# Kernel tuning notes

Hardware: AMD Instinct MI355X
Metric: run time of the kernel (lower is better)

## Reference

```python
import jax, jax.numpy as jnp
import numpy as np

HIDDEN = 1024
HEADS = 16
B, L = 2, 2048


def _xavier(key, shape):
    fan_in, fan_out = shape[1], shape[0]
    limit = float(np.sqrt(6.0 / (fan_in + fan_out)))
    return jax.random.uniform(key, shape, jnp.float32, -limit, limit)


def setup_inputs() -> dict:
    key = jax.random.key(0)
    ks = jax.random.split(key, 6)
    return {
        "query": jax.random.normal(ks[0], (B, L, HIDDEN), jnp.float32),
        "bias": jax.random.normal(ks[1], (B, 1, 1, L), jnp.float32),
        "Wq": _xavier(ks[2], (HIDDEN, HIDDEN)), "bq": jnp.zeros((HIDDEN,), jnp.float32),
        "Wk": _xavier(ks[3], (HIDDEN, HIDDEN)), "bk": jnp.zeros((HIDDEN,), jnp.float32),
        "Wv": _xavier(ks[4], (HIDDEN, HIDDEN)), "bv": jnp.zeros((HIDDEN,), jnp.float32),
        "Wo": _xavier(ks[5], (HIDDEN, HIDDEN)), "bo": jnp.zeros((HIDDEN,), jnp.float32),
    }


def _split_heads(x):
    b, l, c = x.shape
    return x.reshape(b, l, HEADS, c // HEADS).transpose(0, 2, 1, 3)  # [B,H,L,d]


def reference(query, bias, Wq, bq, Wk, bk, Wv, bv, Wo, bo):
    d_head = HIDDEN // HEADS
    q = query @ Wq.T + bq
    k = query @ Wk.T + bk
    v = query @ Wv.T + bv
    q = _split_heads(q) * (d_head ** -0.5)  # [B,H,L,d]
    k = _split_heads(k)
    v = _split_heads(v)
    logits = jnp.einsum("bhqd,bhkd->bhqk", q, k) + bias  # [B,H,L,L]
    weights = jax.nn.softmax(logits, axis=-1)
    x = jnp.einsum("bhqk,bhkd->bhqd", weights, v)  # [B,H,L,d]
    x = x.transpose(0, 2, 1, 3).reshape(query.shape[0], query.shape[1], HIDDEN)
    return x @ Wo.T + bo
```

## Files before the change

### kernel.cpp

```cpp
#include <hip/hip_runtime.h>
#include <hip/hip_fp16.h>
#include <stdint.h>

#define HIDDEN 1024
#define HEADS  16
#define DH     64
#define B_     2
#define L_     2048
#define M_TOT  (B_ * L_)
#define ELEMS  (M_TOT * HIDDEN)
#define LOG2E  1.44269504088896340736f

typedef _Float16 f16;
typedef _Float16 f16x4 __attribute__((ext_vector_type(4)));
typedef _Float16 f16x8 __attribute__((ext_vector_type(8)));
typedef float    f32x4 __attribute__((ext_vector_type(4)));
typedef uint32_t u32;
typedef __attribute__((address_space(1))) u32 gu32;
typedef __attribute__((address_space(3))) u32 su32;

#define MFMA32(a, b, c) __builtin_amdgcn_mfma_f32_16x16x32_f16(a, b, c, 0, 0, 0)


__global__ __launch_bounds__(256)
void convert_f16(const float* __restrict__ query,
                 const float* __restrict__ Wq, const float* __restrict__ Wk,
                 const float* __restrict__ Wv, const float* __restrict__ Wo,
                 f16* __restrict__ Qh, f16* __restrict__ Wh)
{
    const int NQ4 = ELEMS / 4;
    const int NW4 = (HIDDEN * HIDDEN) / 4;
    const int total = NQ4 + 4 * NW4;
    for (int u = blockIdx.x * 256 + threadIdx.x; u < total; u += gridDim.x * 256) {
        float4 v; f16* dp;
        if (u < NQ4) {
            v = ((const float4*)query)[u];
            dp = Qh + (size_t)u * 4;
        } else {
            const int u2 = u - NQ4;
            const int w = u2 >> 18;
            const int off = u2 & (NW4 - 1);
            const float* W = (w == 0) ? Wq : (w == 1) ? Wk : (w == 2) ? Wv : Wo;
            v = ((const float4*)W)[off];
            dp = Wh + (size_t)u2 * 4;
        }
        f16x4 h = { (f16)v.x, (f16)v.y, (f16)v.z, (f16)v.w };
        *(f16x4*)dp = h;
    }
}

template<int TM, int TN>
__device__ __forceinline__
void gemm_loop(const f16* __restrict__ A, const f16* __restrict__ W,
               int mb, int nb, f32x4 (&acc)[TM / 32][TN / 32])
{
    __shared__ f16 As[3][TM * 32];
    __shared__ f16 Bs[3][TN * 32];

    const int tid  = threadIdx.x;
    const int lane = tid & 63;
    const int wave = tid >> 6;
    const int quad = lane >> 4;
    const int l16  = lane & 15;
    const int wm   = (wave >> 1) * (TM / 2);
    const int wn   = (wave & 1) * (TN / 2);

    constexpr int AISS = TM / 64;
    constexpr int BISS = TN / 64;
    int aoff[AISS], boff[BISS];
#pragma unroll
    for (int q = 0; q < AISS; q++) {
        const int p16 = (wave * AISS + q) * 64 + lane;
        const int r = p16 >> 2;
        const int c8 = (p16 & 3) ^ ((r >> 1) & 3);
        aoff[q] = (mb + r) * HIDDEN + c8 * 8;
    }
#pragma unroll
    for (int q = 0; q < BISS; q++) {
        const int p16 = (wave * BISS + q) * 64 + lane;
        const int r = p16 >> 2;
        const int c8 = (p16 & 3) ^ ((r >> 1) & 3);
        boff[q] = (nb + r) * HIDDEN + c8 * 8;
    }

#pragma unroll
    for (int p = 0; p < 2; p++) {
#pragma unroll
        for (int q = 0; q < AISS; q++)
            __builtin_amdgcn_global_load_lds((gu32*)&A[aoff[q] + p * 32],
                                             (su32*)&As[p][(wave * AISS + q) * 512], 16, 0, 0);
#pragma unroll
        for (int q = 0; q < BISS; q++)
            __builtin_amdgcn_global_load_lds((gu32*)&W[boff[q] + p * 32],
                                             (su32*)&Bs[p][(wave * BISS + q) * 512], 16, 0, 0);
    }

    int sl = 0;
#pragma unroll 1
    for (int kb = 0; kb < HIDDEN; kb += 32) {
        if constexpr (AISS + BISS == 4)
            asm volatile("s_waitcnt vmcnt(4)" ::: "memory");
        else
            asm volatile("s_waitcnt vmcnt(3)" ::: "memory");
        __builtin_amdgcn_s_barrier();
        __builtin_amdgcn_sched_barrier(0);

        const int nkb = (kb + 64 < HIDDEN) ? kb + 64 : 0;
        const int si  = (sl >= 1) ? sl - 1 : 2;
#pragma unroll
        for (int q = 0; q < AISS; q++)
            __builtin_amdgcn_global_load_lds((gu32*)&A[aoff[q] + nkb],
                                             (su32*)&As[si][(wave * AISS + q) * 512], 16, 0, 0);
#pragma unroll
        for (int q = 0; q < BISS; q++)
            __builtin_amdgcn_global_load_lds((gu32*)&W[boff[q] + nkb],
                                             (su32*)&Bs[si][(wave * BISS + q) * 512], 16, 0, 0);

        f16x8 af[TM / 32], bf[TN / 32];
#pragma unroll
        for (int i = 0; i < TM / 32; i++) {
            const int r = wm + i * 16 + l16;
            af[i] = *(const f16x8*)&As[sl][r * 32 + (quad ^ ((r >> 1) & 3)) * 8];
        }
#pragma unroll
        for (int j = 0; j < TN / 32; j++) {
            const int r = wn + j * 16 + l16;
            bf[j] = *(const f16x8*)&Bs[sl][r * 32 + (quad ^ ((r >> 1) & 3)) * 8];
        }
#pragma unroll
        for (int i = 0; i < TM / 32; i++)
#pragma unroll
            for (int j = 0; j < TN / 32; j++)
                acc[i][j] = MFMA32(af[i], bf[j], acc[i][j]);

        sl = (sl + 1 == 3) ? 0 : sl + 1;
    }
    asm volatile("s_waitcnt vmcnt(0)" ::: "memory");
}

__global__ __launch_bounds__(256)
void proj_qkv(const f16* __restrict__ A, const f16* __restrict__ W,
              const float* __restrict__ bq, const float* __restrict__ bk,
              const float* __restrict__ bv,
              f16* __restrict__ Qo, f16* __restrict__ Ko, f16* __restrict__ Vo)
{
    f32x4 acc[4][4] = {};
    const int mb = blockIdx.x * 128, nb = blockIdx.y * 128;
    gemm_loop<128, 128>(A, W, mb, nb, acc);

    const int lane = threadIdx.x & 63, wave = threadIdx.x >> 6;
    const int quad = lane >> 4, l16 = lane & 15;
    const int wm = (wave >> 1) * 64, wn = (wave & 1) * 64;
    const int nsel = nb >> 10;
    const int nbase = nb & 1023;

    if (nsel < 2) {
        const float* bias = nsel ? bk : bq;
        f16* out = nsel ? Ko : Qo;
        const float scale = nsel ? 1.0f : 0.125f * LOG2E;
#pragma unroll
        for (int i = 0; i < 4; i++)
#pragma unroll
            for (int j = 0; j < 4; j++) {
                const int n1 = nbase + wn + j * 16 + l16;
                const float bn = bias[n1];
                const int h = n1 >> 6, dd = n1 & 63;
#pragma unroll
                for (int r = 0; r < 4; r++) {
                    const int m = mb + wm + i * 16 + quad * 4 + r;
                    const int b = m >> 11, l = m & (L_ - 1);
                    out[(((b * HEADS + h) * L_) + l) * DH + dd] =
                        (f16)((acc[i][j][r] + bn) * scale);
                }
            }
    } else {
#pragma unroll
        for (int i = 0; i < 4; i++)
#pragma unroll
            for (int j = 0; j < 4; j++) {
                const int n1 = nbase + wn + j * 16 + l16;
                const float bn = bv[n1];
                const int h = n1 >> 6, dd = n1 & 63;
                const int m0 = mb + wm + i * 16 + quad * 4;
                const int b = m0 >> 11, l0 = m0 & (L_ - 1);
                f16x4 pk;
#pragma unroll
                for (int r = 0; r < 4; r++) pk[r] = (f16)(acc[i][j][r] + bn);
                *(f16x4*)&Vo[((size_t)(b * HEADS + h) * DH + dd) * L_ + l0] = pk;
            }
    }
}

__global__ __launch_bounds__(256)
void proj_out(const f16* __restrict__ A, const f16* __restrict__ W,
              const float* __restrict__ bo, float* __restrict__ out)
{
    f32x4 acc[4][2] = {};
    const int mb = blockIdx.x * 128, nb = blockIdx.y * 64;
    gemm_loop<128, 64>(A, W, mb, nb, acc);

    const int lane = threadIdx.x & 63, wave = threadIdx.x >> 6;
    const int quad = lane >> 4, l16 = lane & 15;
    const int wm = (wave >> 1) * 64, wn = (wave & 1) * 32;
#pragma unroll
    for (int i = 0; i < 4; i++)
#pragma unroll
        for (int j = 0; j < 2; j++) {
            const int n = nb + wn + j * 16 + l16;
            const float bn = bo[n];
#pragma unroll
            for (int r = 0; r < 4; r++) {
                const int m = mb + wm + i * 16 + quad * 4 + r;
                out[m * HIDDEN + n] = acc[i][j][r] + bn;
            }
        }
}

__global__ __launch_bounds__(256)
void attn(const f16* __restrict__ Q, const f16* __restrict__ K,
          const f16* __restrict__ Vt, const float* __restrict__ bias,
          f16* __restrict__ X)
{
    __shared__ f16 Ks[2][64 * 64];
    __shared__ f16 Vs[2][64 * 64];
    __shared__ float biasl[L_];

    const int tid  = threadIdx.x;
    const int lane = tid & 63;
    const int wave = tid >> 6;
    const int quad = lane >> 4;
    const int l16  = lane & 15;

    const int bid = (int)blockIdx.x;
    const int lb  = (bid & 7) * 128 + (bid >> 3);
    const int bh = lb >> 5;
    const int b  = bh >> 4, h = bh & 15;
    const int qrow0 = (lb & 31) * 64 + wave * 16;

    const f16* Qh  = Q  + (size_t)bh * L_ * DH;
    const f16* Kh  = K  + (size_t)bh * L_ * DH;
    const f16* Vth = Vt + (size_t)bh * DH * L_;

    {
        const float4* bb = (const float4*)(bias + b * L_);
        for (int i = tid; i < L_ / 4; i += 256) {
            const float4 v = bb[i];
            biasl[i * 4 + 0] = v.x * LOG2E;
            biasl[i * 4 + 1] = v.y * LOG2E;
            biasl[i * 4 + 2] = v.z * LOG2E;
            biasl[i * 4 + 3] = v.w * LOG2E;
        }
    }

    int krow[2], kcol[2], vcol[2];
#pragma unroll
    for (int q = 0; q < 2; q++) {
        const int p = (wave * 2 + q) * 64 + lane;
        const int r = p >> 3;
        const int w = p & 7;
        krow[q] = r;
        kcol[q] = (w ^ (r & 7) ^ (((r >> 3) & 1) << 2)) * 8;
        vcol[q] = (w ^ (r & 7)) * 8;
    }

    f16x8 qf[2];
#pragma unroll
    for (int hh = 0; hh < 2; hh++)
        qf[hh] = *(const f16x8*)&Qh[(qrow0 + l16) * DH + hh * 32 + quad * 8];

    int koffX[2][2], koffY[2][2], voff[2][4];
#pragma unroll
    for (int g = 0; g < 2; g++) {
        const int rX = g * 32 + ((l16 >> 2) << 3) + (l16 & 3);
        const int rY = rX + 4;
        const int gkX = (rX & 7) ^ (((rX >> 3) & 1) << 2);
        const int gkY = (rY & 7) ^ (((rY >> 3) & 1) << 2);
#pragma unroll
        for (int hh = 0; hh < 2; hh++) {
            koffX[g][hh] = rX * 64 + (((hh * 4 + quad) ^ gkX) << 3);
            koffY[g][hh] = rY * 64 + (((hh * 4 + quad) ^ gkY) << 3);
        }
#pragma unroll
        for (int t = 0; t < 4; t++) {
            const int vr = t * 16 + l16;
            voff[g][t] = vr * 64 + (((g * 4 + quad) ^ (vr & 7)) << 3);
        }
    }

#pragma unroll
    for (int q = 0; q < 2; q++) {
        __builtin_amdgcn_global_load_lds((gu32*)(Kh + (size_t)krow[q] * DH + kcol[q]),
                                         (su32*)&Ks[0][(wave * 2 + q) * 512], 16, 0, 0);
        __builtin_amdgcn_global_load_lds((gu32*)(Vth + (size_t)krow[q] * L_ + vcol[q]),
                                         (su32*)&Vs[0][(wave * 2 + q) * 512], 16, 0, 0);
    }

    f32x4 o[4] = {};
    f32x4 osum = {};
    const f16x8 ones8 = { (f16)1.f, (f16)1.f, (f16)1.f, (f16)1.f,
                          (f16)1.f, (f16)1.f, (f16)1.f, (f16)1.f };
    __syncthreads();

#pragma unroll 1
    for (int kb = 0; kb < L_; kb += 64) {
        const int buf = (kb >> 6) & 1;
        const int nkb = (kb + 64 < L_) ? kb + 64 : 0;

#pragma unroll
        for (int q = 0; q < 2; q++) {
            __builtin_amdgcn_global_load_lds(
                (gu32*)(Kh + (size_t)(nkb + krow[q]) * DH + kcol[q]),
                (su32*)&Ks[buf ^ 1][(wave * 2 + q) * 512], 16, 0, 0);
            __builtin_amdgcn_global_load_lds(
                (gu32*)(Vth + (size_t)krow[q] * L_ + nkb + vcol[q]),
                (su32*)&Vs[buf ^ 1][(wave * 2 + q) * 512], 16, 0, 0);
        }

#pragma unroll
        for (int g = 0; g < 2; g++) {
            const f16x8 kx0 = *(const f16x8*)&Ks[buf][koffX[g][0]];
            const f16x8 kx1 = *(const f16x8*)&Ks[buf][koffX[g][1]];
            const f16x8 ky0 = *(const f16x8*)&Ks[buf][koffY[g][0]];
            const f16x8 ky1 = *(const f16x8*)&Ks[buf][koffY[g][1]];
            f16x8 va[4];
#pragma unroll
            for (int t = 0; t < 4; t++)
                va[t] = *(const f16x8*)&Vs[buf][voff[g][t]];
            const f32x4 blvX = *(const f32x4*)&biasl[kb + g * 32 + quad * 8];
            const f32x4 blvY = *(const f32x4*)&biasl[kb + g * 32 + quad * 8 + 4];

            f32x4 zx = blvX, zy = blvY;
            zx = MFMA32(kx0, qf[0], zx);
            zx = MFMA32(kx1, qf[1], zx);
            zy = MFMA32(ky0, qf[0], zy);
            zy = MFMA32(ky1, qf[1], zy);
            const f16x8 pb = {
                (f16)__builtin_amdgcn_exp2f(zx[0]), (f16)__builtin_amdgcn_exp2f(zx[1]),
                (f16)__builtin_amdgcn_exp2f(zx[2]), (f16)__builtin_amdgcn_exp2f(zx[3]),
                (f16)__builtin_amdgcn_exp2f(zy[0]), (f16)__builtin_amdgcn_exp2f(zy[1]),
                (f16)__builtin_amdgcn_exp2f(zy[2]), (f16)__builtin_amdgcn_exp2f(zy[3]) };
#pragma unroll
            for (int t = 0; t < 4; t++)
                o[t] = MFMA32(va[t], pb, o[t]);
            osum = MFMA32(ones8, pb, osum);
        }
        __syncthreads();
    }

    {
        const float inv = 1.0f / osum[0];
        const size_t qrow = (size_t)b * L_ + qrow0 + l16;
#pragma unroll
        for (int t = 0; t < 4; t++) {
            f16x4 pk;
#pragma unroll
            for (int r = 0; r < 4; r++) pk[r] = (f16)(o[t][r] * inv);
            *(f16x4*)&X[qrow * HIDDEN + h * DH + t * 16 + quad * 4] = pk;
        }
    }
}

extern "C" void kernel_launch(void* const* d_in, const int* in_sizes, int n_in,
                              void* d_out, int out_size, void* d_ws, size_t ws_size,
                              hipStream_t stream)
{
    const float* query = (const float*)d_in[0];
    const float* bias  = (const float*)d_in[1];
    const float* Wq = (const float*)d_in[2]; const float* bq = (const float*)d_in[3];
    const float* Wk = (const float*)d_in[4]; const float* bk = (const float*)d_in[5];
    const float* Wv = (const float*)d_in[6]; const float* bv = (const float*)d_in[7];
    const float* Wo = (const float*)d_in[8]; const float* bo = (const float*)d_in[9];
    float* out = (float*)d_out;

    f16* Wh = (f16*)d_ws;
    f16* Qh = Wh + 4096 * 1024;
    f16* Kf = Qh + ELEMS;
    f16* Vf = Kf + ELEMS;
    f16* Qf = Vf + ELEMS;
    f16* Xf = Qh;

    convert_f16<<<2048, 256, 0, stream>>>(query, Wq, Wk, Wv, Wo, Qh, Wh);
    proj_qkv<<<dim3(32, 24), 256, 0, stream>>>(Qh, Wh, bq, bk, bv, Qf, Kf, Vf);
    attn<<<1024, 256, 0, stream>>>(Qf, Kf, Vf, bias, Xf);
    proj_out<<<dim3(32, 16), 256, 0, stream>>>(Xf, Wh + 3072 * 1024, bo, out);
}
```

Before: 201.4 us.

## Split attention keys across wave pairs with 2 query tiles each; vectorize GEMM epilogues

```diff
diff --git a/kernel.cpp b/kernel.cpp
--- a/kernel.cpp
+++ b/kernel.cpp
@@ -49,7 +49,7 @@
     }
 }
 
-template<int TM, int TN>
+template<int TM, int TN, bool SWAP>
 __device__ __forceinline__
 void gemm_loop(const f16* __restrict__ A, const f16* __restrict__ W,
                int mb, int nb, f32x4 (&acc)[TM / 32][TN / 32])
@@ -130,8 +130,12 @@
 #pragma unroll
         for (int i = 0; i < TM / 32; i++)
 #pragma unroll
-            for (int j = 0; j < TN / 32; j++)
-                acc[i][j] = MFMA32(af[i], bf[j], acc[i][j]);
+            for (int j = 0; j < TN / 32; j++) {
+                if constexpr (SWAP)
+                    acc[i][j] = MFMA32(bf[j], af[i], acc[i][j]);
+                else
+                    acc[i][j] = MFMA32(af[i], bf[j], acc[i][j]);
+            }
 
         sl = (sl + 1 == 3) ? 0 : sl + 1;
     }
@@ -146,12 +150,13 @@
 {
     f32x4 acc[4][4] = {};
     const int mb = blockIdx.x * 128, nb = blockIdx.y * 128;
-    gemm_loop<128, 128>(A, W, mb, nb, acc);
+    const int nsel = nb >> 10;
+    if (nsel < 2) gemm_loop<128, 128, true >(A, W, mb, nb, acc);
+    else          gemm_loop<128, 128, false>(A, W, mb, nb, acc);
 
     const int lane = threadIdx.x & 63, wave = threadIdx.x >> 6;
     const int quad = lane >> 4, l16 = lane & 15;
     const int wm = (wave >> 1) * 64, wn = (wave & 1) * 64;
-    const int nsel = nb >> 10;
     const int nbase = nb & 1023;
 
     if (nsel < 2) {
@@ -159,20 +164,21 @@
         f16* out = nsel ? Ko : Qo;
         const float scale = nsel ? 1.0f : 0.125f * LOG2E;
 #pragma unroll
-        for (int i = 0; i < 4; i++)
+        for (int i = 0; i < 4; i++) {
+            const int m = mb + wm + i * 16 + l16;
+            const int b = m >> 11, l = m & (L_ - 1);
 #pragma unroll
             for (int j = 0; j < 4; j++) {
-                const int n1 = nbase + wn + j * 16 + l16;
-                const float bn = bias[n1];
-                const int h = n1 >> 6, dd = n1 & 63;
-#pragma unroll
-                for (int r = 0; r < 4; r++) {
-                    const int m = mb + wm + i * 16 + quad * 4 + r;
-                    const int b = m >> 11, l = m & (L_ - 1);
-                    out[(((b * HEADS + h) * L_) + l) * DH + dd] =
-                        (f16)((acc[i][j][r] + bn) * scale);
-                }
-            }
+                const int n0 = nbase + wn + j * 16 + quad * 4;
+                const f32x4 bl4 = *(const f32x4*)&bias[n0];
+                const int h = n0 >> 6, dd = n0 & 63;
+                f16x4 pk;
+#pragma unroll
+                for (int r = 0; r < 4; r++)
+                    pk[r] = (f16)((acc[i][j][r] + bl4[r]) * scale);
+                *(f16x4*)&out[(((b * HEADS + h) * L_) + l) * DH + dd] = pk;
+            }
+        }
     } else {
 #pragma unroll
         for (int i = 0; i < 4; i++)
@@ -197,26 +203,29 @@
 {
     f32x4 acc[4][2] = {};
     const int mb = blockIdx.x * 128, nb = blockIdx.y * 64;
-    gemm_loop<128, 64>(A, W, mb, nb, acc);
+    gemm_loop<128, 64, true>(A, W, mb, nb, acc);
 
     const int lane = threadIdx.x & 63, wave = threadIdx.x >> 6;
     const int quad = lane >> 4, l16 = lane & 15;
     const int wm = (wave >> 1) * 64, wn = (wave & 1) * 32;
 #pragma unroll
-    for (int i = 0; i < 4; i++)
+    for (int i = 0; i < 4; i++) {
+        const int m = mb + wm + i * 16 + l16;
 #pragma unroll
         for (int j = 0; j < 2; j++) {
-            const int n = nb + wn + j * 16 + l16;
-            const float bn = bo[n];
-#pragma unroll
-            for (int r = 0; r < 4; r++) {
-                const int m = mb + wm + i * 16 + quad * 4 + r;
-                out[m * HIDDEN + n] = acc[i][j][r] + bn;
-            }
-        }
-}
-
-__global__ __launch_bounds__(256)
+            const int n0 = nb + wn + j * 16 + quad * 4;
+            const float4 b4 = *(const float4*)&bo[n0];
+            float4 st;
+            st.x = acc[i][j][0] + b4.x;
+            st.y = acc[i][j][1] + b4.y;
+            st.z = acc[i][j][2] + b4.z;
+            st.w = acc[i][j][3] + b4.w;
+            *(float4*)&out[m * HIDDEN + n0] = st;
+        }
+    }
+}
+
+__global__ __launch_bounds__(512, 4)
 void attn(const f16* __restrict__ Q, const f16* __restrict__ K,
           const f16* __restrict__ Vt, const float* __restrict__ bias,
           f16* __restrict__ X)
@@ -230,73 +239,69 @@
     const int wave = tid >> 6;
     const int quad = lane >> 4;
     const int l16  = lane & 15;
+    const int qg   = wave >> 1;
+    const int g    = wave & 1;
 
     const int bid = (int)blockIdx.x;
-    const int lb  = (bid & 7) * 128 + (bid >> 3);
-    const int bh = lb >> 5;
-    const int b  = bh >> 4, h = bh & 15;
-    const int qrow0 = (lb & 31) * 64 + wave * 16;
+    const int lb  = (bid & 7) * 64 + (bid >> 3);
+    const int bh  = lb >> 4;
+    const int b   = bh >> 4, h = bh & 15;
+    const int qrow0 = (lb & 15) * 128 + qg * 32;
 
     const f16* Qh  = Q  + (size_t)bh * L_ * DH;
     const f16* Kh  = K  + (size_t)bh * L_ * DH;
     const f16* Vth = Vt + (size_t)bh * DH * L_;
 
     {
-        const float4* bb = (const float4*)(bias + b * L_);
-        for (int i = tid; i < L_ / 4; i += 256) {
-            const float4 v = bb[i];
-            biasl[i * 4 + 0] = v.x * LOG2E;
-            biasl[i * 4 + 1] = v.y * LOG2E;
-            biasl[i * 4 + 2] = v.z * LOG2E;
-            biasl[i * 4 + 3] = v.w * LOG2E;
-        }
-    }
-
-    int krow[2], kcol[2], vcol[2];
-#pragma unroll
-    for (int q = 0; q < 2; q++) {
-        const int p = (wave * 2 + q) * 64 + lane;
+        const float4 v = ((const float4*)(bias + b * L_))[tid];
+        biasl[tid * 4 + 0] = v.x * LOG2E;
+        biasl[tid * 4 + 1] = v.y * LOG2E;
+        biasl[tid * 4 + 2] = v.z * LOG2E;
+        biasl[tid * 4 + 3] = v.w * LOG2E;
+    }
+
+    int krow, kcol, vcol;
+    {
+        const int p = wave * 64 + lane;
         const int r = p >> 3;
-        const int w = p & 7;
-        krow[q] = r;
-        kcol[q] = (w ^ (r & 7) ^ (((r >> 3) & 1) << 2)) * 8;
-        vcol[q] = (w ^ (r & 7)) * 8;
-    }
-
-    f16x8 qf[2];
-#pragma unroll
-    for (int hh = 0; hh < 2; hh++)
-        qf[hh] = *(const f16x8*)&Qh[(qrow0 + l16) * DH + hh * 32 + quad * 8];
-
-    int koffX[2][2], koffY[2][2], voff[2][4];
-#pragma unroll
-    for (int g = 0; g < 2; g++) {
+        const int w8 = p & 7;
+        krow = r;
+        kcol = (w8 ^ (r & 7) ^ (((r >> 3) & 1) << 2)) * 8;
+        vcol = (w8 ^ (r & 7)) * 8;
+    }
+
+    f16x8 qf[2][2];
+#pragma unroll
+    for (int qt = 0; qt < 2; qt++)
+#pragma unroll
+        for (int hh = 0; hh < 2; hh++)
+            qf[qt][hh] = *(const f16x8*)&Qh[(qrow0 + qt * 16 + l16) * DH + hh * 32 + quad * 8];
+
+    int koffX[2], koffY[2], voff[4];
+    {
         const int rX = g * 32 + ((l16 >> 2) << 3) + (l16 & 3);
         const int rY = rX + 4;
         const int gkX = (rX & 7) ^ (((rX >> 3) & 1) << 2);
         const int gkY = (rY & 7) ^ (((rY >> 3) & 1) << 2);
 #pragma unroll
         for (int hh = 0; hh < 2; hh++) {
-            koffX[g][hh] = rX * 64 + (((hh * 4 + quad) ^ gkX) << 3);
-            koffY[g][hh] = rY * 64 + (((hh * 4 + quad) ^ gkY) << 3);
+            koffX[hh] = rX * 64 + (((hh * 4 + quad) ^ gkX) << 3);
+            koffY[hh] = rY * 64 + (((hh * 4 + quad) ^ gkY) << 3);
         }
 #pragma unroll
         for (int t = 0; t < 4; t++) {
             const int vr = t * 16 + l16;
-            voff[g][t] = vr * 64 + (((g * 4 + quad) ^ (vr & 7)) << 3);
-        }
-    }
-
-#pragma unroll
-    for (int q = 0; q < 2; q++) {
-        __builtin_amdgcn_global_load_lds((gu32*)(Kh + (size_t)krow[q] * DH + kcol[q]),
-                                         (su32*)&Ks[0][(wave * 2 + q) * 512], 16, 0, 0);
-        __builtin_amdgcn_global_load_lds((gu32*)(Vth + (size_t)krow[q] * L_ + vcol[q]),
-                                         (su32*)&Vs[0][(wave * 2 + q) * 512], 16, 0, 0);
-    }
-
-    f32x4 o[4] = {};
-    f32x4 osum = {};
+            voff[t] = vr * 64 + (((g * 4 + quad) ^ (vr & 7)) << 3);
+        }
+    }
+
+    __builtin_amdgcn_global_load_lds((gu32*)(Kh + (size_t)krow * DH + kcol),
+                                     (su32*)&Ks[0][wave * 512], 16, 0, 0);
+    __builtin_amdgcn_global_load_lds((gu32*)(Vth + (size_t)krow * L_ + vcol),
+                                     (su32*)&Vs[0][wave * 512], 16, 0, 0);
+
+    f32x4 o[2][4] = {};
+    f32x4 osum[2] = {};
     const f16x8 ones8 = { (f16)1.f, (f16)1.f, (f16)1.f, (f16)1.f,
                           (f16)1.f, (f16)1.f, (f16)1.f, (f16)1.f };
     __syncthreads();
@@ -306,34 +311,31 @@
         const int buf = (kb >> 6) & 1;
         const int nkb = (kb + 64 < L_) ? kb + 64 : 0;
 
-#pragma unroll
-        for (int q = 0; q < 2; q++) {
-            __builtin_amdgcn_global_load_lds(
-                (gu32*)(Kh + (size_t)(nkb + krow[q]) * DH + kcol[q]),
-                (su32*)&Ks[buf ^ 1][(wave * 2 + q) * 512], 16, 0, 0);
-            __builtin_amdgcn_global_load_lds(
-                (gu32*)(Vth + (size_t)krow[q] * L_ + nkb + vcol[q]),
-                (su32*)&Vs[buf ^ 1][(wave * 2 + q) * 512], 16, 0, 0);
-        }
-
-#pragma unroll
-        for (int g = 0; g < 2; g++) {
-            const f16x8 kx0 = *(const f16x8*)&Ks[buf][koffX[g][0]];
-            const f16x8 kx1 = *(const f16x8*)&Ks[buf][koffX[g][1]];
-            const f16x8 ky0 = *(const f16x8*)&Ks[buf][koffY[g][0]];
-            const f16x8 ky1 = *(const f16x8*)&Ks[buf][koffY[g][1]];
-            f16x8 va[4];
-#pragma unroll
-            for (int t = 0; t < 4; t++)
-                va[t] = *(const f16x8*)&Vs[buf][voff[g][t]];
-            const f32x4 blvX = *(const f32x4*)&biasl[kb + g * 32 + quad * 8];
-            const f32x4 blvY = *(const f32x4*)&biasl[kb + g * 32 + quad * 8 + 4];
-
+        __builtin_amdgcn_global_load_lds(
+            (gu32*)(Kh + (size_t)(nkb + krow) * DH + kcol),
+            (su32*)&Ks[buf ^ 1][wave * 512], 16, 0, 0);
+        __builtin_amdgcn_global_load_lds(
+            (gu32*)(Vth + (size_t)krow * L_ + nkb + vcol),
+            (su32*)&Vs[buf ^ 1][wave * 512], 16, 0, 0);
+
+        const f16x8 kx0 = *(const f16x8*)&Ks[buf][koffX[0]];
+        const f16x8 kx1 = *(const f16x8*)&Ks[buf][koffX[1]];
+        const f16x8 ky0 = *(const f16x8*)&Ks[buf][koffY[0]];
+        const f16x8 ky1 = *(const f16x8*)&Ks[buf][koffY[1]];
+        f16x8 va[4];
+#pragma unroll
+        for (int t = 0; t < 4; t++)
+            va[t] = *(const f16x8*)&Vs[buf][voff[t]];
+        const f32x4 blvX = *(const f32x4*)&biasl[kb + g * 32 + quad * 8];
+        const f32x4 blvY = *(const f32x4*)&biasl[kb + g * 32 + quad * 8 + 4];
+
+#pragma unroll
+        for (int qt = 0; qt < 2; qt++) {
             f32x4 zx = blvX, zy = blvY;
-            zx = MFMA32(kx0, qf[0], zx);
-            zx = MFMA32(kx1, qf[1], zx);
-            zy = MFMA32(ky0, qf[0], zy);
-            zy = MFMA32(ky1, qf[1], zy);
+            zx = MFMA32(kx0, qf[qt][0], zx);
+            zx = MFMA32(kx1, qf[qt][1], zx);
+            zy = MFMA32(ky0, qf[qt][0], zy);
+            zy = MFMA32(ky1, qf[qt][1], zy);
             const f16x8 pb = {
                 (f16)__builtin_amdgcn_exp2f(zx[0]), (f16)__builtin_amdgcn_exp2f(zx[1]),
                 (f16)__builtin_amdgcn_exp2f(zx[2]), (f16)__builtin_amdgcn_exp2f(zx[3]),
@@ -341,21 +343,47 @@
                 (f16)__builtin_amdgcn_exp2f(zy[2]), (f16)__builtin_amdgcn_exp2f(zy[3]) };
 #pragma unroll
             for (int t = 0; t < 4; t++)
-                o[t] = MFMA32(va[t], pb, o[t]);
-            osum = MFMA32(ones8, pb, osum);
+                o[qt][t] = MFMA32(va[t], pb, o[qt][t]);
+            osum[qt] = MFMA32(ones8, pb, osum[qt]);
         }
         __syncthreads();
     }
 
-    {
-        const float inv = 1.0f / osum[0];
-        const size_t qrow = (size_t)b * L_ + qrow0 + l16;
-#pragma unroll
-        for (int t = 0; t < 4; t++) {
-            f16x4 pk;
-#pragma unroll
-            for (int r = 0; r < 4; r++) pk[r] = (f16)(o[t][r] * inv);
-            *(f16x4*)&X[qrow * HIDDEN + h * DH + t * 16 + quad * 4] = pk;
+    float* o0 = (float*)Ks;
+    float* o1 = (float*)Vs;
+    if (g) {
+#pragma unroll
+        for (int t = 0; t < 4; t++)
+#pragma unroll
+            for (int r = 0; r < 4; r++) {
+                o0[(qg * 16 + t * 4 + r) * 64 + lane] = o[0][t][r];
+                o1[(qg * 16 + t * 4 + r) * 64 + lane] = o[1][t][r];
+            }
+        biasl[(qg * 64 + lane) * 2 + 0] = osum[0][0];
+        biasl[(qg * 64 + lane) * 2 + 1] = osum[1][0];
+    }
+    __syncthreads();
+    if (!g) {
+#pragma unroll
+        for (int t = 0; t < 4; t++)
+#pragma unroll
+            for (int r = 0; r < 4; r++) {
+                o[0][t][r] += o0[(qg * 16 + t * 4 + r) * 64 + lane];
+                o[1][t][r] += o1[(qg * 16 + t * 4 + r) * 64 + lane];
+            }
+        const float s0 = osum[0][0] + biasl[(qg * 64 + lane) * 2 + 0];
+        const float s1 = osum[1][0] + biasl[(qg * 64 + lane) * 2 + 1];
+#pragma unroll
+        for (int qt = 0; qt < 2; qt++) {
+            const float inv = 1.0f / (qt ? s1 : s0);
+            const size_t qrow = (size_t)b * L_ + qrow0 + qt * 16 + l16;
+#pragma unroll
+            for (int t = 0; t < 4; t++) {
+                f16x4 pk;
+#pragma unroll
+                for (int r = 0; r < 4; r++) pk[r] = (f16)(o[qt][t][r] * inv);
+                *(f16x4*)&X[qrow * HIDDEN + h * DH + t * 16 + quad * 4] = pk;
+            }
         }
     }
 }
@@ -381,6 +409,6 @@
 
     convert_f16<<<2048, 256, 0, stream>>>(query, Wq, Wk, Wv, Wo, Qh, Wh);
     proj_qkv<<<dim3(32, 24), 256, 0, stream>>>(Qh, Wh, bq, bk, bv, Qf, Kf, Vf);
-    attn<<<1024, 256, 0, stream>>>(Qf, Kf, Vf, bias, Xf);
+    attn<<<512, 512, 0, stream>>>(Qf, Kf, Vf, bias, Xf);
     proj_out<<<dim3(32, 16), 256, 0, stream>>>(Xf, Wh + 3072 * 1024, bo, out);
 }
```

After: 222.9 us. 10.7% more time.
